# Performance work log

Hardware: AMD Instinct MI355X
Metric: run time of the kernel (lower is better)

The kernel has to match this reference:

```python
import jax, jax.numpy as jnp
import numpy as np

Z, H, W = 8, 96, 192
WZ, WH, WW = 2, 6, 12
C, HEADS, DEPTH, B = 192, 6, 2, 1
NZ, NH, NW = Z // WZ, H // WH, W // WW
LW = WZ * WH * WW            # 144 tokens per window
WIN_TYPES = NZ * NH          # 64 earth-specific window types
NPOS = WZ * WZ * WH * WH * (2 * WW - 1)  # 3312 relative-position entries
HD = C // HEADS
SCALE = HD ** -0.5
SZ, SH, SW = WZ // 2, WH // 2, WW // 2


def _position_index():
    czi = np.arange(WZ); czj = -np.arange(WZ) * WZ
    chi = np.arange(WH); chj = -np.arange(WH) * WH
    cw = np.arange(WW)
    c1 = np.stack(np.meshgrid(czi, chi, cw, indexing='ij'), 0).reshape(3, -1)
    c2 = np.stack(np.meshgrid(czj, chj, cw, indexing='ij'), 0).reshape(3, -1)
    coords = (c1[:, :, None] - c2[:, None, :]).transpose(1, 2, 0).astype(np.int64).copy()
    coords[:, :, 2] += WW - 1
    coords[:, :, 1] *= 2 * WW - 1
    coords[:, :, 0] *= (2 * WW - 1) * WH * WH
    return coords.sum(-1).reshape(-1)


def _attention_mask():
    m = np.zeros((Z, H, W))
    zs = (slice(0, -WZ), slice(-WZ, -SZ), slice(-SZ, None))
    hs = (slice(0, -WH), slice(-WH, -SH), slice(-SH, None))
    ws = (slice(0, -WW), slice(-WW, -SW), slice(-SW, None))
    cnt = 0
    for z in zs:
        for h in hs:
            for w in ws:
                m[z, h, w] = cnt
                cnt += 1
    mw = m.reshape(NZ, WZ, NH, WH, NW, WW).transpose(0, 2, 4, 1, 3, 5).reshape(-1, LW)
    d = mw[:, None, :] - mw[:, :, None]
    return np.where(d != 0, -100.0, 0.0).astype(np.float32)


def setup_inputs() -> dict:
    key = jax.random.key(0)
    ks = jax.random.split(key, 12)
    s = 0.02
    def rn(k, shape):
        return jax.random.normal(k, shape, jnp.float32) * s
    return {
        'x': jax.random.normal(ks[0], (B, Z * H * W, C), jnp.float32),
        'qkv_w': rn(ks[1], (DEPTH, C, 3 * C)),
        'qkv_b': rn(ks[2], (DEPTH, 3 * C)),
        'proj_w': rn(ks[3], (DEPTH, C, C)),
        'proj_b': rn(ks[4], (DEPTH, C)),
        'bias_tab': rn(ks[5], (DEPTH, NPOS, WIN_TYPES, HEADS)),
        'n1_g': jnp.ones((DEPTH, C), jnp.float32),
        'n1_b': jnp.zeros((DEPTH, C), jnp.float32),
        'n2_g': jnp.ones((DEPTH, C), jnp.float32),
        'n2_b': jnp.zeros((DEPTH, C), jnp.float32),
        'mlp_w1': rn(ks[6], (DEPTH, C, 4 * C)),
        'mlp_b1': rn(ks[7], (DEPTH, 4 * C)),
        'mlp_w2': rn(ks[8], (DEPTH, 4 * C, C)),
        'mlp_b2': rn(ks[9], (DEPTH, C)),
        'pos_index': jnp.asarray(_position_index(), jnp.int32),
        'attn_mask': jnp.asarray(_attention_mask()),
    }


def _ln(x, g, b):
    m = x.mean(-1, keepdims=True)
    v = jnp.mean((x - m) ** 2, -1, keepdims=True)
    return (x - m) / jnp.sqrt(v + 1e-5) * g + b


def _forward(x, qkv_w, qkv_b, proj_w, proj_b, bias_tab, n1_g, n1_b, n2_g, n2_b,
             mlp_w1, mlp_b1, mlp_w2, mlp_b2, pos_index, attn_mask):
    for blk in range(DEPTH):
        roll = (blk % 2 == 1)
        shortcut = x
        h = _ln(x, n1_g[blk], n1_b[blk]).reshape(B, Z, H, W, C)
        if roll:
            h = jnp.roll(h, (-SZ, -SH, -SW), (1, 2, 3))
        # partition windows: (B*nZ*nH*nW, LW, C)
        h = h.reshape(B, NZ, WZ, NH, WH, NW, WW, C).transpose(0, 1, 3, 5, 2, 4, 6, 7).reshape(-1, LW, C)
        B_ = h.shape[0]
        qkv = (h @ qkv_w[blk] + qkv_b[blk]).reshape(B_, LW, 3, HEADS, HD)
        q = qkv[:, :, 0].transpose(0, 2, 1, 3) * SCALE  # (B_, heads, LW, hd)
        k = qkv[:, :, 1].transpose(0, 2, 1, 3)
        v = qkv[:, :, 2].transpose(0, 2, 1, 3)
        attn = jnp.einsum('bhid,bhjd->bhij', q, k)
        # earth-specific bias gathered by relative-position index
        bias = bias_tab[blk][pos_index].reshape(LW, LW, WIN_TYPES, HEADS).transpose(2, 3, 0, 1)
        attn = (attn.reshape(-1, WIN_TYPES, HEADS, LW, LW) + bias).reshape(B_, HEADS, LW, LW)
        if roll:
            attn = (attn.reshape(B, WIN_TYPES * NW, HEADS, LW, LW) + attn_mask[None, :, None]).reshape(B_, HEADS, LW, LW)
        attn = jax.nn.softmax(attn, -1)
        o = jnp.einsum('bhij,bhjd->bhid', attn, v).transpose(0, 2, 1, 3).reshape(B_, LW, C)
        o = o @ proj_w[blk] + proj_b[blk]
        # reverse windows
        o = o.reshape(B, NZ, NH, NW, WZ, WH, WW, C).transpose(0, 1, 4, 2, 5, 3, 6, 7).reshape(B, Z, H, W, C)
        if roll:
            o = jnp.roll(o, (SZ, SH, SW), (1, 2, 3))
        x = shortcut + o.reshape(B, Z * H * W, C)
        h2 = _ln(x, n2_g[blk], n2_b[blk])
        h2 = jax.nn.gelu(h2 @ mlp_w1[blk] + mlp_b1[blk], approximate=False) @ mlp_w2[blk] + mlp_b2[blk]
        x = x + h2
    return x


def reference(x, qkv_w, qkv_b, proj_w, proj_b, bias_tab, n1_g, n1_b, n2_g, n2_b,
              mlp_w1, mlp_b1, mlp_w2, mlp_b2, pos_index, attn_mask):
    return _forward(x, qkv_w, qkv_b, proj_w, proj_b, bias_tab, n1_g, n1_b, n2_g, n2_b,
                    mlp_w1, mlp_b1, mlp_w2, mlp_b2, pos_index, attn_mask)
```

## Files before the change

### kernel.cpp

```cpp
#include <hip/hip_runtime.h>
#include <math.h>

#define TZ 8
#define TH 96
#define TW 192
#define C 192
#define NHEADS 6
#define HDIM 32
#define LW 144
#define NWIN 1024
#define NTOK 147456
#define NPOS 3312
#define QSCALE 0.17677669529663687f

typedef unsigned short u16;
typedef __attribute__((ext_vector_type(8))) short bf8_t;
typedef __attribute__((ext_vector_type(4))) short bf4_t;
typedef __attribute__((ext_vector_type(4))) unsigned short us4_t;
typedef __attribute__((ext_vector_type(4))) float f4_t;

__device__ __forceinline__ float bf2f(u16 u) {
    union { unsigned int i; float f; } c; c.i = ((unsigned int)u) << 16; return c.f;
}
__device__ __forceinline__ u16 f2bf(float f) {
    union { float f; unsigned int i; } c; c.f = f;
    unsigned int x = c.i;
    x += 0x7fffu + ((x >> 16) & 1u);
    return (u16)(x >> 16);
}

__device__ __forceinline__ int win_row_to_token(int r, int roll) {
    int wi = r / LW, l = r % LW;
    int nz = wi >> 8, nh = (wi >> 4) & 15, nw = wi & 15;
    int iz = l / 72, rr = l % 72, ih = rr / 12, iw = rr % 12;
    int z = nz * 2 + iz, h = nh * 6 + ih, w = nw * 12 + iw;
    if (roll) {
        z = (z + 1) & 7;
        h += 3; if (h >= TH) h -= TH;
        w += 6; if (w >= TW) w -= TW;
    }
    return (z * TH + h) * TW + w;
}

__global__ __launch_bounds__(256) void ln_kernel(
    const float* __restrict__ x, const float* __restrict__ g,
    const float* __restrict__ b, u16* __restrict__ xnc,
    int row0, int windowed, int roll)
{
    int wave = threadIdx.x >> 6;
    int lane = threadIdx.x & 63;
    int dl = blockIdx.x * 4 + wave;
    int d = row0 + dl;
    int src = windowed ? win_row_to_token(d, roll) : d;
    const float* xr = x + (size_t)src * C;
    float v0 = xr[lane], v1 = xr[lane + 64], v2 = xr[lane + 128];
    float s = v0 + v1 + v2;
    float sq = v0 * v0 + v1 * v1 + v2 * v2;
    #pragma unroll
    for (int off = 32; off > 0; off >>= 1) {
        s  += __shfl_xor(s, off, 64);
        sq += __shfl_xor(sq, off, 64);
    }
    float mean = s * (1.0f / 192.0f);
    float var  = sq * (1.0f / 192.0f) - mean * mean;
    float rstd = rsqrtf(var + 1e-5f);
    u16* orow = xnc + (size_t)dl * C;
    orow[lane]       = f2bf((v0 - mean) * rstd * g[lane]       + b[lane]);
    orow[lane + 64]  = f2bf((v1 - mean) * rstd * g[lane + 64]  + b[lane + 64]);
    orow[lane + 128] = f2bf((v2 - mean) * rstd * g[lane + 128] + b[lane + 128]);
}

__global__ __launch_bounds__(256) void tconv_kernel(
    const float* __restrict__ W, u16* __restrict__ WT, int K, int N)
{
    int idx = blockIdx.x * 256 + threadIdx.x;
    if (idx >= N * K) return;
    int n = idx / K, k = idx % K;
    WT[idx] = f2bf(W[(size_t)k * N + n]);
}

__global__ __launch_bounds__(256) void biasmat_kernel(
    const float* __restrict__ btab, const int* __restrict__ pidx,
    u16* __restrict__ biasf)
{
    int wt = blockIdx.x, head = blockIdx.y;
    size_t obase = ((size_t)wt * 6 + head) * (LW * LW);
    for (int idx = threadIdx.x; idx < LW * LW; idx += 256) {
        int p = pidx[idx];
        biasf[obase + idx] = f2bf(btab[((size_t)p * 64 + wt) * 6 + head]);
    }
}

template <int MODE>
__global__ __launch_bounds__(256) void mm_kernel(
    const u16* __restrict__ A, const u16* __restrict__ BT,
    const float* __restrict__ bias, void* __restrict__ Cvoid,
    int N, int K, int row0, int roll)
{
    __shared__ alignas(16) u16 As[128 * 72];
    __shared__ alignas(16) u16 Bs[64 * 72];
    int tid = threadIdx.x;
    int mb = blockIdx.y * 128, nb = blockIdx.x * 64;
    int wave = tid >> 6, lane = tid & 63;
    int mh = wave >> 1, nh = wave & 1;
    int lr = lane & 15, g = lane >> 4;

    f4_t acc[4][2];
    #pragma unroll
    for (int mi = 0; mi < 4; mi++)
        #pragma unroll
        for (int ni = 0; ni < 2; ni++)
            acc[mi][ni] = (f4_t){0.f, 0.f, 0.f, 0.f};

    for (int k0 = 0; k0 < K; k0 += 64) {
        #pragma unroll
        for (int it = 0; it < 4; it++) {
            int idx = it * 256 + tid;
            int r = idx >> 3, kc = idx & 7;
            *(bf8_t*)&As[r * 72 + kc * 8] =
                *(const bf8_t*)&A[(size_t)(mb + r) * K + k0 + kc * 8];
        }
        #pragma unroll
        for (int it = 0; it < 2; it++) {
            int idx = it * 256 + tid;
            int r = idx >> 3, kc = idx & 7;
            *(bf8_t*)&Bs[r * 72 + kc * 8] =
                *(const bf8_t*)&BT[(size_t)(nb + r) * K + k0 + kc * 8];
        }
        __syncthreads();
        #pragma unroll
        for (int ks = 0; ks < 2; ks++) {
            bf8_t bfr[2];
            #pragma unroll
            for (int ni = 0; ni < 2; ni++)
                bfr[ni] = *(const bf8_t*)&Bs[(nh * 32 + ni * 16 + lr) * 72 + ks * 32 + g * 8];
            #pragma unroll
            for (int mi = 0; mi < 4; mi++) {
                bf8_t afr = *(const bf8_t*)&As[(mh * 64 + mi * 16 + lr) * 72 + ks * 32 + g * 8];
                #pragma unroll
                for (int ni = 0; ni < 2; ni++)
                    acc[mi][ni] = __builtin_amdgcn_mfma_f32_16x16x32_bf16(
                        afr, bfr[ni], acc[mi][ni], 0, 0, 0);
            }
        }
        __syncthreads();
    }

    #pragma unroll
    for (int mi = 0; mi < 4; mi++) {
        int rbase = mb + mh * 64 + mi * 16 + g * 4;
        int tok[4];
        if (MODE == 1) {
            #pragma unroll
            for (int r = 0; r < 4; r++)
                tok[r] = win_row_to_token(row0 + rbase + r, roll);
        }
        #pragma unroll
        for (int ni = 0; ni < 2; ni++) {
            int col = nb + nh * 32 + ni * 16 + lr;
            float bb = bias[col];
            #pragma unroll
            for (int r = 0; r < 4; r++) {
                float v = acc[mi][ni][r] + bb;
                if (MODE == 0) {
                    if (col < 192) v *= QSCALE;
                    ((u16*)Cvoid)[(size_t)(rbase + r) * 576 + col] = f2bf(v);
                } else if (MODE == 1) {
                    ((float*)Cvoid)[(size_t)tok[r] * C + col] += v;
                } else if (MODE == 2) {
                    v = 0.5f * v * (1.0f + erff(v * 0.70710678118654752f));
                    ((u16*)Cvoid)[(size_t)(rbase + r) * 768 + col] = f2bf(v);
                } else {
                    ((float*)Cvoid)[(size_t)(row0 + rbase + r) * C + col] += v;
                }
            }
        }
    }
}

__global__ __launch_bounds__(192, 4) void attn_kernel(
    const u16* __restrict__ qkvb, const u16* __restrict__ biasf,
    u16* __restrict__ attnb, int win0, int roll)
{
    __shared__ alignas(16) u16 Qs[144 * 40];
    __shared__ alignas(16) u16 Ks[144 * 40];
    __shared__ alignas(16) u16 Vt[32 * 148];
    __shared__ unsigned char region8[144];

    int wl = blockIdx.x, head = blockIdx.y;
    int wi = win0 + wl, wt = wi & 63;
    int tid = threadIdx.x;

    const u16* base = qkvb + (size_t)wl * LW * 576;
    for (int c = tid; c < 576; c += 192) {
        int l = c >> 2, d8 = (c & 3) << 3;
        const u16* row = base + (size_t)l * 576 + head * 32;
        *(bf8_t*)&Qs[l * 40 + d8] = *(const bf8_t*)&row[d8];
        *(bf8_t*)&Ks[l * 40 + d8] = *(const bf8_t*)&row[192 + d8];
        bf8_t v8 = *(const bf8_t*)&row[384 + d8];
        #pragma unroll
        for (int m = 0; m < 8; m++)
            Vt[(d8 + m) * 148 + l] = (u16)v8[m];
    }
    if (tid < 144) {
        int nz = wi >> 8, nh = (wi >> 4) & 15, nw = wi & 15;
        int iz = tid / 72, rr = tid % 72, ih = rr / 12, iw = rr % 12;
        int z = nz * 2 + iz, h = nh * 6 + ih, w = nw * 12 + iw;
        int rz = (z < 6) ? 0 : ((z < 7) ? 1 : 2);
        int rh = (h < 90) ? 0 : ((h < 93) ? 1 : 2);
        int rw2 = (w < 180) ? 0 : ((w < 186) ? 1 : 2);
        region8[tid] = (unsigned char)(rz * 9 + rh * 3 + rw2);
    }
    __syncthreads();

    int wave = tid >> 6, lane = tid & 63;
    int lr = lane & 15, g = lane >> 4;
    int jb = g << 2;
    const f4_t z4 = {0.f, 0.f, 0.f, 0.f};

    for (int itl = 0; itl < 3; itl++) {
        int it = wave * 3 + itl;
        int i_row = it * 16 + lr;
        bf8_t qf = *(const bf8_t*)&Qs[i_row * 40 + (g << 3)];
        f4_t s[9];
        #pragma unroll
        for (int jt = 0; jt < 9; jt++) {
            bf8_t kf = *(const bf8_t*)&Ks[(jt * 16 + lr) * 40 + (g << 3)];
            s[jt] = __builtin_amdgcn_mfma_f32_16x16x32_bf16(kf, qf, z4, 0, 0, 0);
        }

        const u16* bb = biasf + ((size_t)(wt * 6 + head) * LW + i_row) * LW;
        unsigned int ri = region8[i_row];
        float m4[4] = {-1e30f, -1e30f, -1e30f, -1e30f};
        #pragma unroll
        for (int jt = 0; jt < 9; jt++) {
            us4_t b4 = *(const us4_t*)&bb[jt * 16 + jb];
            unsigned int rj = 0;
            if (roll) rj = *(const unsigned int*)&region8[jt * 16 + jb];
            #pragma unroll
            for (int r = 0; r < 4; r++) {
                float v = s[jt][r] + bf2f(b4[r]);
                if (roll && (((rj >> (8 * r)) & 255u) != ri)) v -= 100.0f;
                s[jt][r] = v;
                m4[r] = fmaxf(m4[r], v);
            }
        }
        float m = fmaxf(fmaxf(m4[0], m4[1]), fmaxf(m4[2], m4[3]));
        m = fmaxf(m, __shfl_xor(m, 16, 64));
        m = fmaxf(m, __shfl_xor(m, 32, 64));

        float l4[4] = {0.f, 0.f, 0.f, 0.f};
        #pragma unroll
        for (int jt = 0; jt < 9; jt++)
            #pragma unroll
            for (int r = 0; r < 4; r++) {
                float p = __expf(s[jt][r] - m);
                s[jt][r] = p;
                l4[r] += p;
            }
        float lsum = (l4[0] + l4[1]) + (l4[2] + l4[3]);
        lsum += __shfl_xor(lsum, 16, 64);
        lsum += __shfl_xor(lsum, 32, 64);
        float inv = 1.0f / lsum;

        bf8_t pfrag[5];
        #pragma unroll
        for (int t = 0; t < 4; t++)
            #pragma unroll
            for (int m2 = 0; m2 < 4; m2++) {
                pfrag[t][m2]     = (short)f2bf(s[2 * t][m2] * inv);
                pfrag[t][4 + m2] = (short)f2bf(s[2 * t + 1][m2] * inv);
            }
        #pragma unroll
        for (int m2 = 0; m2 < 4; m2++) {
            pfrag[4][m2]     = (short)f2bf(s[8][m2] * inv);
            pfrag[4][4 + m2] = 0;
        }

        #pragma unroll
        for (int dt = 0; dt < 2; dt++) {
            const u16* vrow = &Vt[(dt * 16 + lr) * 148];
            f4_t acc = z4;
            #pragma unroll
            for (int t = 0; t < 5; t++) {
                bf4_t va = *(const bf4_t*)&vrow[t * 32 + jb];
                bf8_t af;
                #pragma unroll
                for (int m2 = 0; m2 < 4; m2++) af[m2] = va[m2];
                if (t < 4) {
                    bf4_t vb = *(const bf4_t*)&vrow[t * 32 + 16 + jb];
                    #pragma unroll
                    for (int m2 = 0; m2 < 4; m2++) af[4 + m2] = vb[m2];
                } else {
                    #pragma unroll
                    for (int m2 = 0; m2 < 4; m2++) af[4 + m2] = 0;
                }
                acc = __builtin_amdgcn_mfma_f32_16x16x32_bf16(af, pfrag[t], acc, 0, 0, 0);
            }
            us4_t o;
            #pragma unroll
            for (int r = 0; r < 4; r++) o[r] = f2bf(acc[r]);
            *(us4_t*)&attnb[((size_t)wl * LW + i_row) * 192 + head * 32 + dt * 16 + jb] = o;
        }
    }
}

extern "C" void kernel_launch(void* const* d_in, const int* in_sizes, int n_in,
                              void* d_out, int out_size, void* d_ws, size_t ws_size,
                              hipStream_t stream)
{
    (void)in_sizes; (void)n_in; (void)out_size; (void)ws_size;
    const float* x_in   = (const float*)d_in[0];
    const float* qkv_w  = (const float*)d_in[1];
    const float* qkv_b  = (const float*)d_in[2];
    const float* proj_w = (const float*)d_in[3];
    const float* proj_b = (const float*)d_in[4];
    const float* btab   = (const float*)d_in[5];
    const float* n1g    = (const float*)d_in[6];
    const float* n1b    = (const float*)d_in[7];
    const float* n2g    = (const float*)d_in[8];
    const float* n2b    = (const float*)d_in[9];
    const float* w1     = (const float*)d_in[10];
    const float* b1     = (const float*)d_in[11];
    const float* w2     = (const float*)d_in[12];
    const float* b2     = (const float*)d_in[13];
    const int*   pidx   = (const int*)d_in[14];

    float* x   = (float*)d_out;
    u16* biasf = (u16*)d_ws;
    u16* wT    = biasf + (size_t)64 * 6 * LW * LW;
    u16* xnc   = wT + 884736;
    u16* qkvb  = xnc + (size_t)NTOK * C;
    u16* attnb = qkvb + (size_t)NTOK * 576;
    u16* hidb  = qkvb;

    const size_t WBLK = 442368;
    const size_t OQKV = 0, OPROJ = 110592, OW1 = 147456, OW2 = 294912;

    hipMemcpyAsync(x, x_in, (size_t)NTOK * C * sizeof(float),
                   hipMemcpyDeviceToDevice, stream);

    for (int blk = 0; blk < 2; blk++) {
        u16* wb = wT + blk * WBLK;
        tconv_kernel<<<(576 * 192 + 255) / 256, 256, 0, stream>>>(
            qkv_w + (size_t)blk * C * 576, wb + OQKV, C, 576);
        tconv_kernel<<<(192 * 192 + 255) / 256, 256, 0, stream>>>(
            proj_w + (size_t)blk * C * C, wb + OPROJ, C, 192);
        tconv_kernel<<<(768 * 192 + 255) / 256, 256, 0, stream>>>(
            w1 + (size_t)blk * C * 768, wb + OW1, C, 768);
        tconv_kernel<<<(192 * 768 + 255) / 256, 256, 0, stream>>>(
            w2 + (size_t)blk * 768 * C, wb + OW2, 768, 192);
    }

    for (int blk = 0; blk < 2; blk++) {
        int roll = blk & 1;
        u16* wb = wT + blk * WBLK;
        biasmat_kernel<<<dim3(64, 6), 256, 0, stream>>>(
            btab + (size_t)blk * NPOS * 64 * 6, pidx, biasf);
        ln_kernel<<<NTOK / 4, 256, 0, stream>>>(
            x, n1g + blk * C, n1b + blk * C, xnc, 0, 1, roll);
        mm_kernel<0><<<dim3(9, NTOK / 128), 256, 0, stream>>>(
            xnc, wb + OQKV, qkv_b + blk * 576, qkvb, 576, C, 0, roll);
        attn_kernel<<<dim3(NWIN, NHEADS), 192, 0, stream>>>(
            qkvb, biasf, attnb, 0, roll);
        mm_kernel<1><<<dim3(3, NTOK / 128), 256, 0, stream>>>(
            attnb, wb + OPROJ, proj_b + blk * C, x, 192, C, 0, roll);
        ln_kernel<<<NTOK / 4, 256, 0, stream>>>(
            x, n2g + blk * C, n2b + blk * C, xnc, 0, 0, 0);
        mm_kernel<2><<<dim3(12, NTOK / 128), 256, 0, stream>>>(
            xnc, wb + OW1, b1 + blk * 768, hidb, 768, C, 0, 0);
        mm_kernel<3><<<dim3(3, NTOK / 128), 256, 0, stream>>>(
            hidb, wb + OW2, b2 + blk * C, x, 192, 768, 0, 0);
    }
}
```

Baseline: 1.620 ms.

## Restructure window attention to one block per window with a wave per head

The attention kernel now launches one 384-thread block per window, with each of its six waves handling one head over all 144 query rows, instead of one block per (window, head). K fragments are held in registers loaded directly from global memory, and Q is prefetched one tile ahead from global rather than staged in LDS. Only V is transposed into shared memory, for all heads at once. The roll flag becomes a template parameter, and the mask comparison runs only for boundary windows that can actually contain multiple regions. This removes the LDS staging of Q and K and the per-element mask work, but raises register pressure and reduces block-level parallelism.

```diff
diff --git a/kernel.cpp b/kernel.cpp
--- a/kernel.cpp
+++ b/kernel.cpp
@@ -12,6 +12,7 @@
 #define NTOK 147456
 #define NPOS 3312
 #define QSCALE 0.17677669529663687f
+#define VHS 4772
 
 typedef unsigned short u16;
 typedef __attribute__((ext_vector_type(8))) short bf8_t;
@@ -178,72 +179,101 @@
     }
 }
 
-__global__ __launch_bounds__(192, 4) void attn_kernel(
+template <int ROLL>
+__global__ __launch_bounds__(384, 3) void attn_kernel(
     const u16* __restrict__ qkvb, const u16* __restrict__ biasf,
-    u16* __restrict__ attnb, int win0, int roll)
-{
-    __shared__ alignas(16) u16 Qs[144 * 40];
-    __shared__ alignas(16) u16 Ks[144 * 40];
-    __shared__ alignas(16) u16 Vt[32 * 148];
-    __shared__ unsigned char region8[144];
-
-    int wl = blockIdx.x, head = blockIdx.y;
-    int wi = win0 + wl, wt = wi & 63;
+    u16* __restrict__ attnb)
+{
+    __shared__ alignas(16) u16 Vt[6 * VHS];
+    __shared__ unsigned char region8[148];
+
+    int wl = blockIdx.x;
+    int wt = wl & 63;
     int tid = threadIdx.x;
-
     const u16* base = qkvb + (size_t)wl * LW * 576;
-    for (int c = tid; c < 576; c += 192) {
-        int l = c >> 2, d8 = (c & 3) << 3;
-        const u16* row = base + (size_t)l * 576 + head * 32;
-        *(bf8_t*)&Qs[l * 40 + d8] = *(const bf8_t*)&row[d8];
-        *(bf8_t*)&Ks[l * 40 + d8] = *(const bf8_t*)&row[192 + d8];
-        bf8_t v8 = *(const bf8_t*)&row[384 + d8];
+
+    #pragma unroll
+    for (int st = 0; st < 9; st++) {
+        int idx = st * 384 + tid;
+        int l = idx / 24, c = idx % 24;
+        int h = c >> 2, dloc = (c & 3) << 3;
+        bf8_t v8 = *(const bf8_t*)&base[(size_t)l * 576 + 384 + c * 8];
+        u16* dst = &Vt[h * VHS + dloc * 148 + l];
         #pragma unroll
         for (int m = 0; m < 8; m++)
-            Vt[(d8 + m) * 148 + l] = (u16)v8[m];
-    }
-    if (tid < 144) {
-        int nz = wi >> 8, nh = (wi >> 4) & 15, nw = wi & 15;
-        int iz = tid / 72, rr = tid % 72, ih = rr / 12, iw = rr % 12;
-        int z = nz * 2 + iz, h = nh * 6 + ih, w = nw * 12 + iw;
-        int rz = (z < 6) ? 0 : ((z < 7) ? 1 : 2);
-        int rh = (h < 90) ? 0 : ((h < 93) ? 1 : 2);
-        int rw2 = (w < 180) ? 0 : ((w < 186) ? 1 : 2);
-        region8[tid] = (unsigned char)(rz * 9 + rh * 3 + rw2);
+            dst[m * 148] = (u16)v8[m];
+    }
+    bool doMask = false;
+    if (ROLL) {
+        int nz = wl >> 8, nh = (wl >> 4) & 15, nw = wl & 15;
+        doMask = (nz == 3) || (nh == 15) || (nw == 15);
+        if (tid < 144) {
+            int iz = tid / 72, rr = tid % 72, ih = rr / 12, iw = rr % 12;
+            int z = nz * 2 + iz, h = nh * 6 + ih, w = nw * 12 + iw;
+            int rz = (z < 6) ? 0 : ((z < 7) ? 1 : 2);
+            int rh = (h < 90) ? 0 : ((h < 93) ? 1 : 2);
+            int rw2 = (w < 180) ? 0 : ((w < 186) ? 1 : 2);
+            region8[tid] = (unsigned char)(rz * 9 + rh * 3 + rw2);
+        }
     }
     __syncthreads();
 
-    int wave = tid >> 6, lane = tid & 63;
+    int head = tid >> 6, lane = tid & 63;
     int lr = lane & 15, g = lane >> 4;
     int jb = g << 2;
+
+    const u16* kbase = base + 192 + head * 32 + g * 8;
+    bf8_t kf[9];
+    #pragma unroll
+    for (int jt = 0; jt < 9; jt++)
+        kf[jt] = *(const bf8_t*)&kbase[(size_t)(jt * 16 + lr) * 576];
+
+    const u16* qbase = base + head * 32 + g * 8;
+    const u16* vhead = &Vt[head * VHS];
+    const u16* bbb = biasf + (size_t)(wt * 6 + head) * LW * LW + jb;
+    u16* obase = attnb + (size_t)wl * LW * 192 + head * 32 + jb;
+
     const f4_t z4 = {0.f, 0.f, 0.f, 0.f};
-
-    for (int itl = 0; itl < 3; itl++) {
-        int it = wave * 3 + itl;
+    bf8_t qf = *(const bf8_t*)&qbase[(size_t)lr * 576];
+
+    for (int it = 0; it < 9; it++) {
         int i_row = it * 16 + lr;
-        bf8_t qf = *(const bf8_t*)&Qs[i_row * 40 + (g << 3)];
+        us4_t barr[9];
+        const u16* bb = bbb + (size_t)i_row * LW;
+        #pragma unroll
+        for (int jt = 0; jt < 9; jt++) barr[jt] = *(const us4_t*)&bb[jt * 16];
+
         f4_t s[9];
         #pragma unroll
-        for (int jt = 0; jt < 9; jt++) {
-            bf8_t kf = *(const bf8_t*)&Ks[(jt * 16 + lr) * 40 + (g << 3)];
-            s[jt] = __builtin_amdgcn_mfma_f32_16x16x32_bf16(kf, qf, z4, 0, 0, 0);
-        }
-
-        const u16* bb = biasf + ((size_t)(wt * 6 + head) * LW + i_row) * LW;
-        unsigned int ri = region8[i_row];
+        for (int jt = 0; jt < 9; jt++)
+            s[jt] = __builtin_amdgcn_mfma_f32_16x16x32_bf16(kf[jt], qf, z4, 0, 0, 0);
+
+        bf8_t qf_n = qf;
+        if (it < 8) qf_n = *(const bf8_t*)&qbase[(size_t)(i_row + 16) * 576];
+
         float m4[4] = {-1e30f, -1e30f, -1e30f, -1e30f};
-        #pragma unroll
-        for (int jt = 0; jt < 9; jt++) {
-            us4_t b4 = *(const us4_t*)&bb[jt * 16 + jb];
-            unsigned int rj = 0;
-            if (roll) rj = *(const unsigned int*)&region8[jt * 16 + jb];
-            #pragma unroll
-            for (int r = 0; r < 4; r++) {
-                float v = s[jt][r] + bf2f(b4[r]);
-                if (roll && (((rj >> (8 * r)) & 255u) != ri)) v -= 100.0f;
-                s[jt][r] = v;
-                m4[r] = fmaxf(m4[r], v);
-            }
+        if (ROLL && doMask) {
+            unsigned int ri = region8[i_row];
+            #pragma unroll
+            for (int jt = 0; jt < 9; jt++) {
+                unsigned int rj = *(const unsigned int*)&region8[jt * 16 + jb];
+                #pragma unroll
+                for (int r = 0; r < 4; r++) {
+                    float v = s[jt][r] + bf2f(barr[jt][r]);
+                    if (((rj >> (8 * r)) & 255u) != ri) v -= 100.0f;
+                    s[jt][r] = v;
+                    m4[r] = fmaxf(m4[r], v);
+                }
+            }
+        } else {
+            #pragma unroll
+            for (int jt = 0; jt < 9; jt++)
+                #pragma unroll
+                for (int r = 0; r < 4; r++) {
+                    float v = s[jt][r] + bf2f(barr[jt][r]);
+                    s[jt][r] = v;
+                    m4[r] = fmaxf(m4[r], v);
+                }
         }
         float m = fmaxf(fmaxf(m4[0], m4[1]), fmaxf(m4[2], m4[3]));
         m = fmaxf(m, __shfl_xor(m, 16, 64));
@@ -279,7 +309,7 @@
 
         #pragma unroll
         for (int dt = 0; dt < 2; dt++) {
-            const u16* vrow = &Vt[(dt * 16 + lr) * 148];
+            const u16* vrow = vhead + (dt * 16 + lr) * 148;
             f4_t acc = z4;
             #pragma unroll
             for (int t = 0; t < 5; t++) {
@@ -300,8 +330,9 @@
             us4_t o;
             #pragma unroll
             for (int r = 0; r < 4; r++) o[r] = f2bf(acc[r]);
-            *(us4_t*)&attnb[((size_t)wl * LW + i_row) * 192 + head * 32 + dt * 16 + jb] = o;
-        }
+            *(us4_t*)&obase[((size_t)i_row) * 192 + dt * 16] = o;
+        }
+        qf = qf_n;
     }
 }
 
@@ -361,8 +392,10 @@
             x, n1g + blk * C, n1b + blk * C, xnc, 0, 1, roll);
         mm_kernel<0><<<dim3(9, NTOK / 128), 256, 0, stream>>>(
             xnc, wb + OQKV, qkv_b + blk * 576, qkvb, 576, C, 0, roll);
-        attn_kernel<<<dim3(NWIN, NHEADS), 192, 0, stream>>>(
-            qkvb, biasf, attnb, 0, roll);
+        if (roll)
+            attn_kernel<1><<<NWIN, 384, 0, stream>>>(qkvb, biasf, attnb);
+        else
+            attn_kernel<0><<<NWIN, 384, 0, stream>>>(qkvb, biasf, attnb);
         mm_kernel<1><<<dim3(3, NTOK / 128), 256, 0, stream>>>(
             attnb, wb + OPROJ, proj_b + blk * C, x, 192, C, 0, roll);
         ln_kernel<<<NTOK / 4, 256, 0, stream>>>(
```

After: 1.594 ms. Within noise of the previous version (-1.6%).
